# Kernel tuning notes

Hardware: AMD Instinct MI355X
Metric: run time of the kernel (lower is better)

Reference implementation:

```python
import jax, jax.numpy as jnp
import numpy as np

B, S, V, E, H, L = 32, 512, 32000, 256, 512, 48


def setup_inputs() -> dict:
    key = jax.random.key(0)
    ks = jax.random.split(key, 12)
    tokens = jax.random.randint(ks[0], (B, S), 0, V)
    length = jax.random.randint(ks[1], (B,), S // 2, S + 1)
    labels = jax.random.randint(ks[2], (B, S), 0, L)
    embed_table = jax.random.normal(ks[3], (V, E), jnp.float32) * 0.1
    embed_table = embed_table.at[0].set(0.0)  # padding_idx = 0
    # torch LSTM gate order: i, f, g, o ; b = b_ih + b_hh folded together
    w_ih_f = jax.random.normal(ks[4], (4 * H, E), jnp.float32) * 0.05
    w_hh_f = jax.random.normal(ks[5], (4 * H, H), jnp.float32) * 0.05
    b_f = jnp.zeros((4 * H,), jnp.float32)
    w_ih_b = jax.random.normal(ks[6], (4 * H, E), jnp.float32) * 0.05
    w_hh_b = jax.random.normal(ks[7], (4 * H, H), jnp.float32) * 0.05
    b_b = jnp.zeros((4 * H,), jnp.float32)
    w_em = jax.random.normal(ks[8], (L, 2 * H), jnp.float32) * 0.02
    b_em = jnp.zeros((L,), jnp.float32)
    transition = jax.random.uniform(ks[9], (L, L), jnp.float32)  # torch.rand init
    return {"tokens": tokens, "length": length, "labels": labels,
            "embed_table": embed_table,
            "w_ih_f": w_ih_f, "w_hh_f": w_hh_f, "b_f": b_f,
            "w_ih_b": w_ih_b, "w_hh_b": w_hh_b, "b_b": b_b,
            "w_em": w_em, "b_em": b_em, "transition": transition}


def _lstm_dir(x, w_ih, w_hh, b, reverse):
    # x: [B,S,E] -> hidden states [B,S,H]
    xw = jnp.einsum('bse,ge->bsg', x, w_ih) + b  # precompute input projection [B,S,4H]
    if reverse:
        xw = xw[:, ::-1]
    Bn = x.shape[0]
    Hn = w_hh.shape[1]
    h0 = jnp.zeros((Bn, Hn), x.dtype)
    c0 = jnp.zeros((Bn, Hn), x.dtype)

    def step(carry, xt):
        h, c = carry
        gates = xt + h @ w_hh.T  # [B,4H]
        i, f, g, o = jnp.split(gates, 4, axis=-1)
        i = jax.nn.sigmoid(i)
        f = jax.nn.sigmoid(f)
        g = jnp.tanh(g)
        o = jax.nn.sigmoid(o)
        c = f * c + i * g
        h = o * jnp.tanh(c)
        return (h, c), h

    _, hs = jax.lax.scan(step, (h0, c0), jnp.swapaxes(xw, 0, 1))
    hs = jnp.swapaxes(hs, 0, 1)  # [B,S,H]
    if reverse:
        hs = hs[:, ::-1]
    return hs


def reference(tokens, length, labels, embed_table,
              w_ih_f, w_hh_f, b_f, w_ih_b, w_hh_b, b_b,
              w_em, b_em, transition):
    x = embed_table[tokens]                      # [B,S,E]
    hf = _lstm_dir(x, w_ih_f, w_hh_f, b_f, reverse=False)
    hb = _lstm_dir(x, w_ih_b, w_hh_b, b_b, reverse=True)
    h = jnp.concatenate([hf, hb], axis=-1)       # [B,S,2H]
    logits = jnp.einsum('bsh,lh->bsl', h, w_em) + b_em
    e = jnp.exp(logits)                          # emission = exp(linear), as in source
    T = jnp.exp(transition)                      # transition = exp(param), as in source
    Bn, Sn = tokens.shape
    pos = jnp.arange(Sn)[None, :]
    mask = pos < length[:, None]                 # [B,S] valid positions

    # gold path score: sum emissions over valid steps + transitions between them
    em_real = jnp.take_along_axis(e, labels[..., None], axis=-1)[..., 0]  # [B,S]
    real = jnp.sum(em_real * mask, axis=-1)
    trans_real = T[labels[:, :-1], labels[:, 1:]]                          # [B,S-1]
    real = real + jnp.sum(trans_real * mask[:, 1:], axis=-1)

    # forward algorithm, exactly as written in source:
    # alpha_new[k] = logsumexp_l( alpha[k] + T[k,l] + e_t[l] )
    alpha0 = e[:, 0, :]                          # [B,L]

    def step(alpha, inp):
        et, mt = inp                             # [B,L], [B]
        scores = alpha[:, :, None] + T[None, :, :] + et[:, None, :]  # [B,L,L]
        new = jax.nn.logsumexp(scores, axis=-1)
        alpha = jnp.where(mt[:, None], new, alpha)
        return alpha, None

    alpha, _ = jax.lax.scan(step, alpha0,
                            (jnp.swapaxes(e[:, 1:], 0, 1),
                             jnp.swapaxes(mask[:, 1:], 0, 1)))
    sum_score = jax.nn.logsumexp(alpha, axis=-1)  # [B]
    return sum_score - real                       # negative log probability per example
```

## Files before the change

kernel.cpp:

```cpp
#include <hip/hip_runtime.h>
#include <math.h>
#include <stdint.h>

#define Bn 32
#define Sn 512
#define En 256
#define Hn 512
#define Ln 48
#define G4 2048
#define NWG 32
#define SENT16 0x7FFFu

typedef unsigned short u16;
typedef __attribute__((ext_vector_type(8))) __bf16 bf16x8;
typedef __attribute__((ext_vector_type(4))) float f32x4;

__device__ inline float bf2f(u16 u) {
    return __uint_as_float(((unsigned)u) << 16);
}
__device__ inline u16 f2bf(float f) {
    unsigned u = __float_as_uint(f);
    unsigned r = (u + 0x7fffu + ((u >> 16) & 1u)) >> 16;
    return (u16)r;
}
__device__ inline float sigmoidf_(float x) { return 1.f / (1.f + expf(-x)); }
__device__ inline float tanh_fast(float x) { return 2.f / (1.f + expf(-2.f * x)) - 1.f; }

__device__ inline unsigned badMask(f32x4 v) {
    unsigned acc = 0;
    #pragma unroll
    for (int i = 0; i < 4; i++) {
        unsigned d = __float_as_uint(v[i]);
        unsigned x = d ^ 0x7FFF7FFFu;
        acc |= (x - 0x00010001u) & ~x & 0x80008000u;
    }
    return acc;
}

__global__ __launch_bounds__(256) void prep_kernel(
    const int* __restrict__ tokens, const float* __restrict__ embed,
    const float* __restrict__ wihf, const float* __restrict__ wihb,
    const float* __restrict__ whhf, const float* __restrict__ whhb,
    const float* __restrict__ wem, const float* __restrict__ trans,
    u16* __restrict__ xbf, u16* __restrict__ wihf_b, u16* __restrict__ wihb_b,
    u16* __restrict__ whhf_b, u16* __restrict__ whhb_b, u16* __restrict__ wem_b,
    float* __restrict__ expT, float* __restrict__ alphaAcc,
    float* __restrict__ realAcc, unsigned* __restrict__ hf32,
    unsigned* __restrict__ hb32)
{
    size_t idx = (size_t)blockIdx.x * blockDim.x + threadIdx.x;
    size_t stride = (size_t)gridDim.x * blockDim.x;
    for (size_t i = idx; i < (size_t)Bn * Sn * En; i += stride) {
        size_t n = i >> 8; int ee = (int)(i & 255);
        int tok = tokens[n];
        xbf[i] = f2bf(embed[(size_t)tok * En + ee]);
    }
    for (size_t i = idx; i < (size_t)G4 * En; i += stride) {
        wihf_b[i] = f2bf(wihf[i]); wihb_b[i] = f2bf(wihb[i]);
    }
    for (size_t i = idx; i < (size_t)G4 * Hn; i += stride) {
        whhf_b[i] = f2bf(whhf[i]); whhb_b[i] = f2bf(whhb[i]);
    }
    for (size_t i = idx; i < (size_t)Ln * 2 * Hn; i += stride) wem_b[i] = f2bf(wem[i]);
    for (size_t i = idx; i < (size_t)Ln * Ln; i += stride) expT[i] = expf(trans[i]);
    for (size_t i = idx; i < (size_t)Bn * Ln; i += stride) alphaAcc[i] = 0.f;
    for (size_t i = idx; i < (size_t)Bn; i += stride) realAcc[i] = 0.f;
    const unsigned sp = (SENT16 << 16) | SENT16;
    for (size_t i = idx; i < (size_t)Bn * Sn * Hn / 2; i += stride) {
        hf32[i] = sp; hb32[i] = sp;
    }
}

__global__ __launch_bounds__(256) void gemm_xw(
    const u16* __restrict__ xbf, const u16* __restrict__ wihf_b,
    const u16* __restrict__ wihb_b, const float* __restrict__ bias_f,
    const float* __restrict__ bias_b, u16* __restrict__ xw_f, u16* __restrict__ xw_b)
{
    int mb = blockIdx.x, nb = blockIdx.y, dir = blockIdx.z;
    const u16* wih = dir ? wihb_b : wihf_b;
    const float* bias = dir ? bias_b : bias_f;
    u16* xw = dir ? xw_b : xw_f;

    __shared__ u16 At[64 * 136];
    __shared__ u16 Bt[64 * 136];

    int tid = threadIdx.x;
    int w = tid >> 6, lane = tid & 63;
    int lm = lane & 15, lkq = (lane >> 4) * 8;
    int Moff = (w & 1) * 32, Noff = (w >> 1) * 32;

    f32x4 zero = {0.f, 0.f, 0.f, 0.f};
    f32x4 acc[2][2] = {{zero, zero}, {zero, zero}};

    for (int kc = 0; kc < 2; kc++) {
        for (int c = tid; c < 1024; c += 256) {
            int r = c >> 4, cc = (c & 15) * 8;
            *(bf16x8*)&At[r * 136 + cc] =
                *(const bf16x8*)&xbf[((size_t)(mb * 64 + r)) * En + kc * 128 + cc];
            *(bf16x8*)&Bt[r * 136 + cc] =
                *(const bf16x8*)&wih[((size_t)(nb * 64 + r)) * En + kc * 128 + cc];
        }
        __syncthreads();
        #pragma unroll
        for (int ks = 0; ks < 4; ks++) {
            int k = ks * 32 + lkq;
            bf16x8 a0 = *(const bf16x8*)&At[(Moff + lm) * 136 + k];
            bf16x8 a1 = *(const bf16x8*)&At[(Moff + 16 + lm) * 136 + k];
            bf16x8 b0 = *(const bf16x8*)&Bt[(Noff + lm) * 136 + k];
            bf16x8 b1 = *(const bf16x8*)&Bt[(Noff + 16 + lm) * 136 + k];
            acc[0][0] = __builtin_amdgcn_mfma_f32_16x16x32_bf16(a0, b0, acc[0][0], 0, 0, 0);
            acc[0][1] = __builtin_amdgcn_mfma_f32_16x16x32_bf16(a0, b1, acc[0][1], 0, 0, 0);
            acc[1][0] = __builtin_amdgcn_mfma_f32_16x16x32_bf16(a1, b0, acc[1][0], 0, 0, 0);
            acc[1][1] = __builtin_amdgcn_mfma_f32_16x16x32_bf16(a1, b1, acc[1][1], 0, 0, 0);
        }
        __syncthreads();
    }
    #pragma unroll
    for (int mi = 0; mi < 2; mi++)
        #pragma unroll
        for (int ni = 0; ni < 2; ni++)
            #pragma unroll
            for (int reg = 0; reg < 4; reg++) {
                int row = Moff + mi * 16 + (lane >> 4) * 4 + reg;
                int col = Noff + ni * 16 + lm;
                int n = mb * 64 + row;
                int g = nb * 64 + col;
                int t = n & 511, b = n >> 9;
                float v = acc[mi][ni][reg] + bias[g];
                xw[((size_t)t * Bn + b) * G4 + g] = f2bf(v);
            }
}

__global__ __launch_bounds__(512) void lstm_rec(
    const u16* __restrict__ whhf_b, const u16* __restrict__ whhb_b,
    const u16* __restrict__ xw_f, const u16* __restrict__ xw_b,
    u16* __restrict__ hf, u16* __restrict__ hb)
{
    int wg = blockIdx.x;
    int dir = wg >> 5;
    int w = wg & 31;
    const u16* __restrict__ whh = dir ? whhb_b : whhf_b;
    const u16* __restrict__ xw  = dir ? xw_b  : xw_f;
    u16* __restrict__ hbuf = dir ? hb : hf;

    __shared__ u16 Hs[32 * 512];
    __shared__ float Cp[4 * 32 * 17];
    __shared__ u16 hout[32 * 16];

    int tid = threadIdx.x;
    int wv = tid >> 6, lane = tid & 63;
    int lm = lane & 15, kq = lane >> 4;
    int mt = wv & 1, nt = wv >> 1;
    int b = tid >> 4, hc = tid & 15;

    bf16x8 Bf[16];
    {
        const u16* wrow = &whh[((size_t)nt * Hn + (size_t)w * 16 + lm) * Hn];
        #pragma unroll
        for (int ks = 0; ks < 16; ks++)
            Bf[ks] = *(const bf16x8*)&wrow[ks * 32 + kq * 8];
    }

    float c_state = 0.f;
    const f32x4 zero = {0.f, 0.f, 0.f, 0.f};

    for (int it = 0; it < Sn; it++) {
        int t = dir ? (Sn - 1 - it) : it;
        f32x4 acc = zero;

        const u16* xp = &xw[((size_t)t * Bn + b) * G4 + (size_t)w * 16 + hc];
        float xg0 = bf2f(xp[0 * Hn]);
        float xg1 = bf2f(xp[1 * Hn]);
        float xg2 = bf2f(xp[2 * Hn]);
        float xg3 = bf2f(xp[3 * Hn]);

        if (it > 0) {
            int tprev = dir ? (t + 1) : (t - 1);
            const u16* base = &hbuf[((size_t)b * Sn + tprev) * Hn];
            const u16* p0 = base + (hc + 0) * 8;
            const u16* p1 = base + (hc + 16) * 8;
            const u16* p2 = base + (hc + 32) * 8;
            const u16* p3 = base + (hc + 48) * 8;
            f32x4 h0, h1, h2, h3;
            int tries = 0;
            while (true) {
                asm volatile(
                    "global_load_dwordx4 %0, %4, off sc1\n\t"
                    "global_load_dwordx4 %1, %5, off sc1\n\t"
                    "global_load_dwordx4 %2, %6, off sc1\n\t"
                    "global_load_dwordx4 %3, %7, off sc1\n\t"
                    "s_waitcnt vmcnt(0)"
                    : "=v"(h0), "=v"(h1), "=v"(h2), "=v"(h3)
                    : "v"(p0), "v"(p1), "v"(p2), "v"(p3)
                    : "memory");
                if (!(badMask(h0) | badMask(h1) | badMask(h2) | badMask(h3))) break;
                if (++tries > (1 << 16)) break;
            }
            *(f32x4*)&Hs[(b * 64 + ((hc + 0) ^ (b & 7))) * 8] = h0;
            *(f32x4*)&Hs[(b * 64 + ((hc + 16) ^ (b & 7))) * 8] = h1;
            *(f32x4*)&Hs[(b * 64 + ((hc + 32) ^ (b & 7))) * 8] = h2;
            *(f32x4*)&Hs[(b * 64 + ((hc + 48) ^ (b & 7))) * 8] = h3;
            __syncthreads();

            f32x4 aa = zero, ab = zero;
            #pragma unroll
            for (int ks2 = 0; ks2 < 8; ks2++) {
                bf16x8 a0 = *(const bf16x8*)
                    &Hs[((mt * 16 + lm) * 64 + (((2 * ks2) * 4 + kq) ^ (lm & 7))) * 8];
                aa = __builtin_amdgcn_mfma_f32_16x16x32_bf16(a0, Bf[2 * ks2], aa, 0, 0, 0);
                bf16x8 a1 = *(const bf16x8*)
                    &Hs[((mt * 16 + lm) * 64 + (((2 * ks2 + 1) * 4 + kq) ^ (lm & 7))) * 8];
                ab = __builtin_amdgcn_mfma_f32_16x16x32_bf16(a1, Bf[2 * ks2 + 1], ab, 0, 0, 0);
            }
            acc = aa + ab;
        }

        #pragma unroll
        for (int reg = 0; reg < 4; reg++)
            Cp[(nt * 32 + mt * 16 + kq * 4 + reg) * 17 + lm] = acc[reg];
        __syncthreads();

        float g0 = Cp[(0 * 32 + b) * 17 + hc] + xg0;
        float g1 = Cp[(1 * 32 + b) * 17 + hc] + xg1;
        float g2 = Cp[(2 * 32 + b) * 17 + hc] + xg2;
        float g3 = Cp[(3 * 32 + b) * 17 + hc] + xg3;
        float i_ = sigmoidf_(g0);
        float f_ = sigmoidf_(g1);
        float gg = tanh_fast(g2);
        float o_ = sigmoidf_(g3);
        c_state = f_ * c_state + i_ * gg;
        float hv = o_ * tanh_fast(c_state);
        hout[tid] = f2bf(hv);
        __syncthreads();

        if (tid < 64) {
            int bq = lane >> 1, half = lane & 1;
            f32x4 hv8 = *(const f32x4*)&hout[lane * 8];
            u16* sp = &hbuf[((size_t)bq * Sn + t) * Hn + (size_t)w * 16 + half * 8];
            asm volatile("global_store_dwordx4 %0, %1, off sc1"
                         :: "v"(sp), "v"(hv8) : "memory");
        }
    }
}

__global__ __launch_bounds__(256) void emis(
    const u16* __restrict__ hf, const u16* __restrict__ hb,
    const u16* __restrict__ wem_b, const float* __restrict__ bem,
    float* __restrict__ e)
{
    int mb = blockIdx.x;
    int tid = threadIdx.x, wv = tid >> 6, lane = tid & 63;
    int lm = lane & 15, lkq = (lane >> 4) * 8;
    int row = mb * 64 + wv * 16;

    f32x4 zero = {0.f, 0.f, 0.f, 0.f};
    f32x4 acc[3] = {zero, zero, zero};
    for (int ks = 0; ks < 32; ks++) {
        int k = ks * 32 + lkq;
        const u16* hsrc = (ks < 16) ? &hf[(size_t)(row + lm) * Hn + k]
                                    : &hb[(size_t)(row + lm) * Hn + (k - 512)];
        bf16x8 a = *(const bf16x8*)hsrc;
        #pragma unroll
        for (int nt = 0; nt < 3; nt++) {
            bf16x8 bfr = *(const bf16x8*)&wem_b[(size_t)(nt * 16 + lm) * 1024 + k];
            acc[nt] = __builtin_amdgcn_mfma_f32_16x16x32_bf16(a, bfr, acc[nt], 0, 0, 0);
        }
    }
    #pragma unroll
    for (int nt = 0; nt < 3; nt++)
        #pragma unroll
        for (int reg = 0; reg < 4; reg++) {
            int r = row + (lane >> 4) * 4 + reg;
            int col = nt * 16 + lm;
            float lg = acc[nt][reg] + bem[col];
            e[(size_t)r * Ln + col] = expf(lg);
        }
}

__global__ __launch_bounds__(64) void crf_step(
    const float* __restrict__ e, const float* __restrict__ expT,
    const int* __restrict__ labels, const int* __restrict__ lengths,
    float* __restrict__ alphaAcc, float* __restrict__ realAcc)
{
    int bt = blockIdx.x;
    int b = bt >> 9, t = bt & 511;
    __shared__ float er[Ln];
    int tid = threadIdx.x;
    if (tid < Ln) er[tid] = e[(size_t)bt * Ln + tid];
    __syncthreads();
    bool inlen = t < lengths[b];
    if (t >= 1 && inlen && tid < Ln) {
        int i = tid;
        float m = -1e30f;
        for (int j = 0; j < Ln; j++) m = fmaxf(m, expT[i * Ln + j] + er[j]);
        float s = 0.f;
        for (int j = 0; j < Ln; j++) s += expf(expT[i * Ln + j] + er[j] - m);
        atomicAdd(&alphaAcc[b * Ln + i], m + logf(s));
    }
    if (tid == 0 && inlen) {
        int lab = labels[b * Sn + t];
        float r = er[lab];
        if (t >= 1) r += expT[labels[b * Sn + t - 1] * Ln + lab];
        atomicAdd(&realAcc[b], r);
    }
}

__global__ __launch_bounds__(64) void finalize(
    const float* __restrict__ e, const float* __restrict__ alphaAcc,
    const float* __restrict__ realAcc, float* __restrict__ out)
{
    int b = threadIdx.x;
    if (b >= Bn) return;
    float m = -1e30f;
    for (int i = 0; i < Ln; i++) {
        float a = e[((size_t)b * Sn) * Ln + i] + alphaAcc[b * Ln + i];
        m = fmaxf(m, a);
    }
    float s = 0.f;
    for (int i = 0; i < Ln; i++) {
        float a = e[((size_t)b * Sn) * Ln + i] + alphaAcc[b * Ln + i];
        s += expf(a - m);
    }
    out[b] = m + logf(s) - realAcc[b];
}

extern "C" void kernel_launch(void* const* d_in, const int* in_sizes, int n_in,
                              void* d_out, int out_size, void* d_ws, size_t ws_size,
                              hipStream_t stream)
{
    const int*   tokens = (const int*)d_in[0];
    const int*   length = (const int*)d_in[1];
    const int*   labels = (const int*)d_in[2];
    const float* embed  = (const float*)d_in[3];
    const float* wihf   = (const float*)d_in[4];
    const float* whhf   = (const float*)d_in[5];
    const float* bf     = (const float*)d_in[6];
    const float* wihb   = (const float*)d_in[7];
    const float* whhb   = (const float*)d_in[8];
    const float* bbv    = (const float*)d_in[9];
    const float* wem    = (const float*)d_in[10];
    const float* bem    = (const float*)d_in[11];
    const float* trans  = (const float*)d_in[12];
    float* out = (float*)d_out;

    char* p = (char*)d_ws;
    auto take = [&](size_t bytes) -> char* {
        char* q = p;
        p += (bytes + 255) & ~(size_t)255;
        return q;
    };
    u16* xw_f   = (u16*)take((size_t)Sn * Bn * G4 * 2);
    u16* xw_b   = (u16*)take((size_t)Sn * Bn * G4 * 2);
    u16* hf     = (u16*)take((size_t)Bn * Sn * Hn * 2);
    u16* hb     = (u16*)take((size_t)Bn * Sn * Hn * 2);
    u16* xbf    = (u16*)take((size_t)Bn * Sn * En * 2);
    u16* wihf_b = (u16*)take((size_t)G4 * En * 2);
    u16* wihb_b = (u16*)take((size_t)G4 * En * 2);
    u16* whhf_b = (u16*)take((size_t)G4 * Hn * 2);
    u16* whhb_b = (u16*)take((size_t)G4 * Hn * 2);
    u16* wem_b  = (u16*)take((size_t)Ln * 2 * Hn * 2);
    float* e        = (float*)take((size_t)Bn * Sn * Ln * 4);
    float* expT     = (float*)take((size_t)Ln * Ln * 4);
    float* alphaAcc = (float*)take((size_t)Bn * Ln * 4);
    float* realAcc  = (float*)take((size_t)Bn * 4);
    if ((size_t)(p - (char*)d_ws) > ws_size) return;

    prep_kernel<<<4096, 256, 0, stream>>>(tokens, embed, wihf, wihb, whhf, whhb, wem, trans,
                                          xbf, wihf_b, wihb_b, whhf_b, whhb_b, wem_b,
                                          expT, alphaAcc, realAcc,
                                          (unsigned*)hf, (unsigned*)hb);

    dim3 g1(256, 32, 2);
    gemm_xw<<<g1, 256, 0, stream>>>(xbf, wihf_b, wihb_b, bf, bbv, xw_f, xw_b);

    void* ra[] = { (void*)&whhf_b, (void*)&whhb_b, (void*)&xw_f, (void*)&xw_b,
                   (void*)&hf, (void*)&hb };
    hipLaunchCooperativeKernel((const void*)lstm_rec, dim3(2 * NWG), dim3(512), ra, 0, stream);

    emis<<<256, 256, 0, stream>>>(hf, hb, wem_b, bem, e);
    crf_step<<<Bn * Sn, 64, 0, stream>>>(e, expT, labels, length, alphaAcc, realAcc);
    finalize<<<1, 64, 0, stream>>>(e, alphaAcc, realAcc, out);
}
```

Before: 1.890 ms.

## Load MFMA A-fragments of h directly from global, dropping LDS staging and barrier

Changes the hidden-state buffer layout from [B,S,H] to [S,B,H] so each wave can fetch its MFMA A operands for the previous timestep straight from global memory with sixteen offset loads. This removes the LDS staging copy and one __syncthreads per timestep on the serial recurrence path. The emission kernel's output indexing is remapped so the CRF stage still sees [B,S,L]. In exchange each wave issues more global loads per step, some of them redundant across waves, and the spin-poll now checks sixteen vectors.

```diff
diff --git a/kernel.cpp b/kernel.cpp
--- a/kernel.cpp
+++ b/kernel.cpp
@@ -143,7 +143,6 @@
     const u16* __restrict__ xw  = dir ? xw_b  : xw_f;
     u16* __restrict__ hbuf = dir ? hb : hf;
 
-    __shared__ u16 Hs[32 * 512];
     __shared__ float Cp[4 * 32 * 17];
     __shared__ u16 hout[32 * 16];
 
@@ -176,43 +175,58 @@
 
         if (it > 0) {
             int tprev = dir ? (t + 1) : (t - 1);
-            const u16* base = &hbuf[((size_t)b * Sn + tprev) * Hn];
-            const u16* p0 = base + (hc + 0) * 8;
-            const u16* p1 = base + (hc + 16) * 8;
-            const u16* p2 = base + (hc + 32) * 8;
-            const u16* p3 = base + (hc + 48) * 8;
-            f32x4 h0, h1, h2, h3;
+            const u16* ab = &hbuf[((size_t)tprev * Bn + (size_t)(mt * 16 + lm)) * Hn + kq * 8];
+            f32x4 A0, A1, A2, A3, A4, A5, A6, A7, A8, A9, A10, A11, A12, A13, A14, A15;
             int tries = 0;
             while (true) {
                 asm volatile(
-                    "global_load_dwordx4 %0, %4, off sc1\n\t"
-                    "global_load_dwordx4 %1, %5, off sc1\n\t"
-                    "global_load_dwordx4 %2, %6, off sc1\n\t"
-                    "global_load_dwordx4 %3, %7, off sc1\n\t"
+                    "global_load_dwordx4 %0, %16, off sc1\n\t"
+                    "global_load_dwordx4 %1, %16, off offset:64 sc1\n\t"
+                    "global_load_dwordx4 %2, %16, off offset:128 sc1\n\t"
+                    "global_load_dwordx4 %3, %16, off offset:192 sc1\n\t"
+                    "global_load_dwordx4 %4, %16, off offset:256 sc1\n\t"
+                    "global_load_dwordx4 %5, %16, off offset:320 sc1\n\t"
+                    "global_load_dwordx4 %6, %16, off offset:384 sc1\n\t"
+                    "global_load_dwordx4 %7, %16, off offset:448 sc1\n\t"
+                    "global_load_dwordx4 %8, %16, off offset:512 sc1\n\t"
+                    "global_load_dwordx4 %9, %16, off offset:576 sc1\n\t"
+                    "global_load_dwordx4 %10, %16, off offset:640 sc1\n\t"
+                    "global_load_dwordx4 %11, %16, off offset:704 sc1\n\t"
+                    "global_load_dwordx4 %12, %16, off offset:768 sc1\n\t"
+                    "global_load_dwordx4 %13, %16, off offset:832 sc1\n\t"
+                    "global_load_dwordx4 %14, %16, off offset:896 sc1\n\t"
+                    "global_load_dwordx4 %15, %16, off offset:960 sc1\n\t"
                     "s_waitcnt vmcnt(0)"
-                    : "=v"(h0), "=v"(h1), "=v"(h2), "=v"(h3)
-                    : "v"(p0), "v"(p1), "v"(p2), "v"(p3)
-                    : "memory");
-                if (!(badMask(h0) | badMask(h1) | badMask(h2) | badMask(h3))) break;
+                    : "=v"(A0), "=v"(A1), "=v"(A2), "=v"(A3),
+                      "=v"(A4), "=v"(A5), "=v"(A6), "=v"(A7),
+                      "=v"(A8), "=v"(A9), "=v"(A10), "=v"(A11),
+                      "=v"(A12), "=v"(A13), "=v"(A14), "=v"(A15)
+                    : "v"(ab) : "memory");
+                unsigned bad = badMask(A0) | badMask(A1) | badMask(A2) | badMask(A3)
+                             | badMask(A4) | badMask(A5) | badMask(A6) | badMask(A7)
+                             | badMask(A8) | badMask(A9) | badMask(A10) | badMask(A11)
+                             | badMask(A12) | badMask(A13) | badMask(A14) | badMask(A15);
+                if (!bad) break;
                 if (++tries > (1 << 16)) break;
             }
-            *(f32x4*)&Hs[(b * 64 + ((hc + 0) ^ (b & 7))) * 8] = h0;
-            *(f32x4*)&Hs[(b * 64 + ((hc + 16) ^ (b & 7))) * 8] = h1;
-            *(f32x4*)&Hs[(b * 64 + ((hc + 32) ^ (b & 7))) * 8] = h2;
-            *(f32x4*)&Hs[(b * 64 + ((hc + 48) ^ (b & 7))) * 8] = h3;
-            __syncthreads();
-
-            f32x4 aa = zero, ab = zero;
-            #pragma unroll
-            for (int ks2 = 0; ks2 < 8; ks2++) {
-                bf16x8 a0 = *(const bf16x8*)
-                    &Hs[((mt * 16 + lm) * 64 + (((2 * ks2) * 4 + kq) ^ (lm & 7))) * 8];
-                aa = __builtin_amdgcn_mfma_f32_16x16x32_bf16(a0, Bf[2 * ks2], aa, 0, 0, 0);
-                bf16x8 a1 = *(const bf16x8*)
-                    &Hs[((mt * 16 + lm) * 64 + (((2 * ks2 + 1) * 4 + kq) ^ (lm & 7))) * 8];
-                ab = __builtin_amdgcn_mfma_f32_16x16x32_bf16(a1, Bf[2 * ks2 + 1], ab, 0, 0, 0);
-            }
-            acc = aa + ab;
+            f32x4 aa = zero, ab2 = zero;
+            aa  = __builtin_amdgcn_mfma_f32_16x16x32_bf16(*(bf16x8*)&A0,  Bf[0],  aa,  0, 0, 0);
+            ab2 = __builtin_amdgcn_mfma_f32_16x16x32_bf16(*(bf16x8*)&A1,  Bf[1],  ab2, 0, 0, 0);
+            aa  = __builtin_amdgcn_mfma_f32_16x16x32_bf16(*(bf16x8*)&A2,  Bf[2],  aa,  0, 0, 0);
+            ab2 = __builtin_amdgcn_mfma_f32_16x16x32_bf16(*(bf16x8*)&A3,  Bf[3],  ab2, 0, 0, 0);
+            aa  = __builtin_amdgcn_mfma_f32_16x16x32_bf16(*(bf16x8*)&A4,  Bf[4],  aa,  0, 0, 0);
+            ab2 = __builtin_amdgcn_mfma_f32_16x16x32_bf16(*(bf16x8*)&A5,  Bf[5],  ab2, 0, 0, 0);
+            aa  = __builtin_amdgcn_mfma_f32_16x16x32_bf16(*(bf16x8*)&A6,  Bf[6],  aa,  0, 0, 0);
+            ab2 = __builtin_amdgcn_mfma_f32_16x16x32_bf16(*(bf16x8*)&A7,  Bf[7],  ab2, 0, 0, 0);
+            aa  = __builtin_amdgcn_mfma_f32_16x16x32_bf16(*(bf16x8*)&A8,  Bf[8],  aa,  0, 0, 0);
+            ab2 = __builtin_amdgcn_mfma_f32_16x16x32_bf16(*(bf16x8*)&A9,  Bf[9],  ab2, 0, 0, 0);
+            aa  = __builtin_amdgcn_mfma_f32_16x16x32_bf16(*(bf16x8*)&A10, Bf[10], aa,  0, 0, 0);
+            ab2 = __builtin_amdgcn_mfma_f32_16x16x32_bf16(*(bf16x8*)&A11, Bf[11], ab2, 0, 0, 0);
+            aa  = __builtin_amdgcn_mfma_f32_16x16x32_bf16(*(bf16x8*)&A12, Bf[12], aa,  0, 0, 0);
+            ab2 = __builtin_amdgcn_mfma_f32_16x16x32_bf16(*(bf16x8*)&A13, Bf[13], ab2, 0, 0, 0);
+            aa  = __builtin_amdgcn_mfma_f32_16x16x32_bf16(*(bf16x8*)&A14, Bf[14], aa,  0, 0, 0);
+            ab2 = __builtin_amdgcn_mfma_f32_16x16x32_bf16(*(bf16x8*)&A15, Bf[15], ab2, 0, 0, 0);
+            acc = aa + ab2;
         }
 
         #pragma unroll
@@ -236,7 +250,7 @@
         if (tid < 64) {
             int bq = lane >> 1, half = lane & 1;
             f32x4 hv8 = *(const f32x4*)&hout[lane * 8];
-            u16* sp = &hbuf[((size_t)bq * Sn + t) * Hn + (size_t)w * 16 + half * 8];
+            u16* sp = &hbuf[((size_t)t * Bn + bq) * Hn + (size_t)w * 16 + half * 8];
             asm volatile("global_store_dwordx4 %0, %1, off sc1"
                          :: "v"(sp), "v"(hv8) : "memory");
         }
@@ -272,8 +286,9 @@
         for (int reg = 0; reg < 4; reg++) {
             int r = row + (lane >> 4) * 4 + reg;
             int col = nt * 16 + lm;
+            int bb = r & 31, tt = r >> 5;
             float lg = acc[nt][reg] + bem[col];
-            e[(size_t)r * Ln + col] = expf(lg);
+            e[(((size_t)bb << 9) + tt) * Ln + col] = expf(lg);
         }
 }
 
```

New measurement: 3.749 ms. 98.4% more time.

## Halve recurrent LSTM workgroups, each handling 32 hidden units per step

Applied to the files above, without the earlier changes.

The persistent recurrent kernel now uses 16 workgroups per direction instead of 32. Each workgroup owns 32 hidden columns, holds two sets of W_hh fragments in registers and issues twice the MFMAs per step. Fewer workgroups means fewer participants polling each step's h broadcast through global memory, which should cut synchronisation latency. The cost is more register pressure and about twice the per-step compute and gate math per workgroup. The host launch grid must also shrink to match.

```diff
diff --git a/kernel.cpp b/kernel.cpp
--- a/kernel.cpp
+++ b/kernel.cpp
@@ -8,7 +8,7 @@
 #define Hn 512
 #define Ln 48
 #define G4 2048
-#define NWG 32
+#define NWG 16
 #define SENT16 0x7FFFu
 
 typedef unsigned short u16;
@@ -137,15 +137,15 @@
     u16* __restrict__ hf, u16* __restrict__ hb)
 {
     int wg = blockIdx.x;
-    int dir = wg >> 5;
-    int w = wg & 31;
+    int dir = wg >> 4;
+    int w = wg & 15;
     const u16* __restrict__ whh = dir ? whhb_b : whhf_b;
     const u16* __restrict__ xw  = dir ? xw_b  : xw_f;
     u16* __restrict__ hbuf = dir ? hb : hf;
 
     __shared__ u16 Hs[32 * 512];
-    __shared__ float Cp[4 * 32 * 17];
-    __shared__ u16 hout[32 * 16];
+    __shared__ float Cp[4 * 32 * 33];
+    __shared__ u16 hout[32 * 32];
 
     int tid = threadIdx.x;
     int wv = tid >> 6, lane = tid & 63;
@@ -153,26 +153,29 @@
     int mt = wv & 1, nt = wv >> 1;
     int b = tid >> 4, hc = tid & 15;
 
-    bf16x8 Bf[16];
+    bf16x8 Bf0[16], Bf1[16];
     {
-        const u16* wrow = &whh[((size_t)nt * Hn + (size_t)w * 16 + lm) * Hn];
-        #pragma unroll
-        for (int ks = 0; ks < 16; ks++)
-            Bf[ks] = *(const bf16x8*)&wrow[ks * 32 + kq * 8];
-    }
-
-    float c_state = 0.f;
+        const u16* wrow0 = &whh[((size_t)nt * Hn + (size_t)w * 32 + lm) * Hn];
+        const u16* wrow1 = &whh[((size_t)nt * Hn + (size_t)w * 32 + 16 + lm) * Hn];
+        #pragma unroll
+        for (int ks = 0; ks < 16; ks++) {
+            Bf0[ks] = *(const bf16x8*)&wrow0[ks * 32 + kq * 8];
+            Bf1[ks] = *(const bf16x8*)&wrow1[ks * 32 + kq * 8];
+        }
+    }
+
+    float cs0 = 0.f, cs1 = 0.f;
     const f32x4 zero = {0.f, 0.f, 0.f, 0.f};
 
     for (int it = 0; it < Sn; it++) {
         int t = dir ? (Sn - 1 - it) : it;
-        f32x4 acc = zero;
-
-        const u16* xp = &xw[((size_t)t * Bn + b) * G4 + (size_t)w * 16 + hc];
-        float xg0 = bf2f(xp[0 * Hn]);
-        float xg1 = bf2f(xp[1 * Hn]);
-        float xg2 = bf2f(xp[2 * Hn]);
-        float xg3 = bf2f(xp[3 * Hn]);
+        f32x4 acc0 = zero, acc1 = zero;
+
+        const u16* xp = &xw[((size_t)t * Bn + b) * G4 + (size_t)w * 32 + hc];
+        float xgA0 = bf2f(xp[0 * Hn]),      xgB0 = bf2f(xp[0 * Hn + 16]);
+        float xgA1 = bf2f(xp[1 * Hn]),      xgB1 = bf2f(xp[1 * Hn + 16]);
+        float xgA2 = bf2f(xp[2 * Hn]),      xgB2 = bf2f(xp[2 * Hn + 16]);
+        float xgA3 = bf2f(xp[3 * Hn]),      xgB3 = bf2f(xp[3 * Hn + 16]);
 
         if (it > 0) {
             int tprev = dir ? (t + 1) : (t - 1);
@@ -202,41 +205,54 @@
             *(f32x4*)&Hs[(b * 64 + ((hc + 48) ^ (b & 7))) * 8] = h3;
             __syncthreads();
 
-            f32x4 aa = zero, ab = zero;
+            f32x4 aa0 = zero, ab0 = zero, aa1 = zero, ab1 = zero;
             #pragma unroll
             for (int ks2 = 0; ks2 < 8; ks2++) {
                 bf16x8 a0 = *(const bf16x8*)
                     &Hs[((mt * 16 + lm) * 64 + (((2 * ks2) * 4 + kq) ^ (lm & 7))) * 8];
-                aa = __builtin_amdgcn_mfma_f32_16x16x32_bf16(a0, Bf[2 * ks2], aa, 0, 0, 0);
+                aa0 = __builtin_amdgcn_mfma_f32_16x16x32_bf16(a0, Bf0[2 * ks2], aa0, 0, 0, 0);
+                aa1 = __builtin_amdgcn_mfma_f32_16x16x32_bf16(a0, Bf1[2 * ks2], aa1, 0, 0, 0);
                 bf16x8 a1 = *(const bf16x8*)
                     &Hs[((mt * 16 + lm) * 64 + (((2 * ks2 + 1) * 4 + kq) ^ (lm & 7))) * 8];
-                ab = __builtin_amdgcn_mfma_f32_16x16x32_bf16(a1, Bf[2 * ks2 + 1], ab, 0, 0, 0);
+                ab0 = __builtin_amdgcn_mfma_f32_16x16x32_bf16(a1, Bf0[2 * ks2 + 1], ab0, 0, 0, 0);
+                ab1 = __builtin_amdgcn_mfma_f32_16x16x32_bf16(a1, Bf1[2 * ks2 + 1], ab1, 0, 0, 0);
             }
-            acc = aa + ab;
-        }
-
-        #pragma unroll
-        for (int reg = 0; reg < 4; reg++)
-            Cp[(nt * 32 + mt * 16 + kq * 4 + reg) * 17 + lm] = acc[reg];
+            acc0 = aa0 + ab0;
+            acc1 = aa1 + ab1;
+        }
+
+        #pragma unroll
+        for (int reg = 0; reg < 4; reg++) {
+            int r = (nt * 32 + mt * 16 + kq * 4 + reg) * 33;
+            Cp[r + lm] = acc0[reg];
+            Cp[r + 16 + lm] = acc1[reg];
+        }
         __syncthreads();
 
-        float g0 = Cp[(0 * 32 + b) * 17 + hc] + xg0;
-        float g1 = Cp[(1 * 32 + b) * 17 + hc] + xg1;
-        float g2 = Cp[(2 * 32 + b) * 17 + hc] + xg2;
-        float g3 = Cp[(3 * 32 + b) * 17 + hc] + xg3;
-        float i_ = sigmoidf_(g0);
-        float f_ = sigmoidf_(g1);
-        float gg = tanh_fast(g2);
-        float o_ = sigmoidf_(g3);
-        c_state = f_ * c_state + i_ * gg;
-        float hv = o_ * tanh_fast(c_state);
-        hout[tid] = f2bf(hv);
+        float gA0 = Cp[(0 * 32 + b) * 33 + hc] + xgA0;
+        float gA1 = Cp[(1 * 32 + b) * 33 + hc] + xgA1;
+        float gA2 = Cp[(2 * 32 + b) * 33 + hc] + xgA2;
+        float gA3 = Cp[(3 * 32 + b) * 33 + hc] + xgA3;
+        float gB0 = Cp[(0 * 32 + b) * 33 + 16 + hc] + xgB0;
+        float gB1 = Cp[(1 * 32 + b) * 33 + 16 + hc] + xgB1;
+        float gB2 = Cp[(2 * 32 + b) * 33 + 16 + hc] + xgB2;
+        float gB3 = Cp[(3 * 32 + b) * 33 + 16 + hc] + xgB3;
+        float iA = sigmoidf_(gA0), fA = sigmoidf_(gA1);
+        float gA = tanh_fast(gA2), oA = sigmoidf_(gA3);
+        cs0 = fA * cs0 + iA * gA;
+        float hvA = oA * tanh_fast(cs0);
+        float iB = sigmoidf_(gB0), fB = sigmoidf_(gB1);
+        float gB = tanh_fast(gB2), oB = sigmoidf_(gB3);
+        cs1 = fB * cs1 + iB * gB;
+        float hvB = oB * tanh_fast(cs1);
+        hout[b * 32 + hc] = f2bf(hvA);
+        hout[b * 32 + 16 + hc] = f2bf(hvB);
         __syncthreads();
 
-        if (tid < 64) {
-            int bq = lane >> 1, half = lane & 1;
-            f32x4 hv8 = *(const f32x4*)&hout[lane * 8];
-            u16* sp = &hbuf[((size_t)bq * Sn + t) * Hn + (size_t)w * 16 + half * 8];
+        if (tid < 128) {
+            int bq = tid >> 2, part = tid & 3;
+            f32x4 hv8 = *(const f32x4*)&hout[bq * 32 + part * 8];
+            u16* sp = &hbuf[((size_t)bq * Sn + t) * Hn + (size_t)w * 32 + part * 8];
             asm volatile("global_store_dwordx4 %0, %1, off sc1"
                          :: "v"(sp), "v"(hv8) : "memory");
         }
```

Result: no change. 1.918 ms (+1.5%).

## Fuse emission GEMM with CRF step and enlarge xw GEMM tiles

Applied to the files above, without the earlier changes.

The emission kernel now keeps each block's 64 timesteps of emissions in shared memory and computes the CRF logsumexp terms and gold-path scores in place. It reduces these per block before issuing atomics, so the separate 16K-block crf_step launch and the full emission buffer round-trip are gone; only the t=0 emissions are written out for finalize. Separately, the input-projection GEMM moves from 64x64 to 128x128 tiles with a 4x4 MFMA accumulator grid per wave, increasing reuse at the cost of more registers and fewer blocks. These stages are small next to the sequential LSTM recurrence, so the overall effect is likely limited.

```diff
diff --git a/kernel.cpp b/kernel.cpp
--- a/kernel.cpp
+++ b/kernel.cpp
@@ -81,50 +81,61 @@
     const float* bias = dir ? bias_b : bias_f;
     u16* xw = dir ? xw_b : xw_f;
 
-    __shared__ u16 At[64 * 136];
-    __shared__ u16 Bt[64 * 136];
+    __shared__ u16 As[128 * 72];
+    __shared__ u16 Bs[128 * 72];
 
     int tid = threadIdx.x;
     int w = tid >> 6, lane = tid & 63;
-    int lm = lane & 15, lkq = (lane >> 4) * 8;
-    int Moff = (w & 1) * 32, Noff = (w >> 1) * 32;
+    int lm = lane & 15, kq = lane >> 4;
+    int Moff = (w & 1) * 64, Noff = (w >> 1) * 64;
 
     f32x4 zero = {0.f, 0.f, 0.f, 0.f};
-    f32x4 acc[2][2] = {{zero, zero}, {zero, zero}};
-
-    for (int kc = 0; kc < 2; kc++) {
-        for (int c = tid; c < 1024; c += 256) {
-            int r = c >> 4, cc = (c & 15) * 8;
-            *(bf16x8*)&At[r * 136 + cc] =
-                *(const bf16x8*)&xbf[((size_t)(mb * 64 + r)) * En + kc * 128 + cc];
-            *(bf16x8*)&Bt[r * 136 + cc] =
-                *(const bf16x8*)&wih[((size_t)(nb * 64 + r)) * En + kc * 128 + cc];
+    f32x4 acc[4][4];
+    #pragma unroll
+    for (int mi = 0; mi < 4; mi++)
+        #pragma unroll
+        for (int ni = 0; ni < 4; ni++) acc[mi][ni] = zero;
+
+    for (int kc = 0; kc < 4; kc++) {
+        #pragma unroll
+        for (int it = 0; it < 4; it++) {
+            int idx = tid + it * 256;
+            int r = idx >> 3, pos = (idx & 7) * 8;
+            *(bf16x8*)&As[r * 72 + pos] =
+                *(const bf16x8*)&xbf[((size_t)(mb * 128 + r)) * En + kc * 64 + pos];
+            *(bf16x8*)&Bs[r * 72 + pos] =
+                *(const bf16x8*)&wih[((size_t)(nb * 128 + r)) * En + kc * 64 + pos];
         }
         __syncthreads();
         #pragma unroll
-        for (int ks = 0; ks < 4; ks++) {
-            int k = ks * 32 + lkq;
-            bf16x8 a0 = *(const bf16x8*)&At[(Moff + lm) * 136 + k];
-            bf16x8 a1 = *(const bf16x8*)&At[(Moff + 16 + lm) * 136 + k];
-            bf16x8 b0 = *(const bf16x8*)&Bt[(Noff + lm) * 136 + k];
-            bf16x8 b1 = *(const bf16x8*)&Bt[(Noff + 16 + lm) * 136 + k];
-            acc[0][0] = __builtin_amdgcn_mfma_f32_16x16x32_bf16(a0, b0, acc[0][0], 0, 0, 0);
-            acc[0][1] = __builtin_amdgcn_mfma_f32_16x16x32_bf16(a0, b1, acc[0][1], 0, 0, 0);
-            acc[1][0] = __builtin_amdgcn_mfma_f32_16x16x32_bf16(a1, b0, acc[1][0], 0, 0, 0);
-            acc[1][1] = __builtin_amdgcn_mfma_f32_16x16x32_bf16(a1, b1, acc[1][1], 0, 0, 0);
+        for (int ks = 0; ks < 2; ks++) {
+            int k = ks * 32 + kq * 8;
+            bf16x8 af[4], bfr[4];
+            #pragma unroll
+            for (int mi = 0; mi < 4; mi++)
+                af[mi] = *(const bf16x8*)&As[(Moff + mi * 16 + lm) * 72 + k];
+            #pragma unroll
+            for (int ni = 0; ni < 4; ni++)
+                bfr[ni] = *(const bf16x8*)&Bs[(Noff + ni * 16 + lm) * 72 + k];
+            #pragma unroll
+            for (int mi = 0; mi < 4; mi++)
+                #pragma unroll
+                for (int ni = 0; ni < 4; ni++)
+                    acc[mi][ni] = __builtin_amdgcn_mfma_f32_16x16x32_bf16(
+                        af[mi], bfr[ni], acc[mi][ni], 0, 0, 0);
         }
         __syncthreads();
     }
     #pragma unroll
-    for (int mi = 0; mi < 2; mi++)
-        #pragma unroll
-        for (int ni = 0; ni < 2; ni++)
+    for (int mi = 0; mi < 4; mi++)
+        #pragma unroll
+        for (int ni = 0; ni < 4; ni++)
             #pragma unroll
             for (int reg = 0; reg < 4; reg++) {
-                int row = Moff + mi * 16 + (lane >> 4) * 4 + reg;
+                int row = Moff + mi * 16 + kq * 4 + reg;
                 int col = Noff + ni * 16 + lm;
-                int n = mb * 64 + row;
-                int g = nb * 64 + col;
+                int n = mb * 128 + row;
+                int g = nb * 128 + col;
                 int t = n & 511, b = n >> 9;
                 float v = acc[mi][ni][reg] + bias[g];
                 xw[((size_t)t * Bn + b) * G4 + g] = f2bf(v);
@@ -243,13 +254,25 @@
     }
 }
 
-__global__ __launch_bounds__(256) void emis(
+__global__ __launch_bounds__(256) void emis_crf(
     const u16* __restrict__ hf, const u16* __restrict__ hb,
     const u16* __restrict__ wem_b, const float* __restrict__ bem,
-    float* __restrict__ e)
+    const float* __restrict__ expT, const int* __restrict__ labels,
+    const int* __restrict__ lengths, float* __restrict__ e0,
+    float* __restrict__ alphaAcc, float* __restrict__ realAcc)
 {
     int mb = blockIdx.x;
-    int tid = threadIdx.x, wv = tid >> 6, lane = tid & 63;
+    int b = mb >> 3, t0 = (mb & 7) * 64;
+
+    __shared__ float eL[64][49];
+    __shared__ float Ts[48 * 48];
+    __shared__ float sred[4][48];
+    __shared__ float rred[64];
+
+    int tid = threadIdx.x;
+    for (int i = tid; i < 48 * 48; i += 256) Ts[i] = expT[i];
+
+    int wv = tid >> 6, lane = tid & 63;
     int lm = lane & 15, lkq = (lane >> 4) * 8;
     int row = mb * 64 + wv * 16;
 
@@ -270,55 +293,65 @@
     for (int nt = 0; nt < 3; nt++)
         #pragma unroll
         for (int reg = 0; reg < 4; reg++) {
-            int r = row + (lane >> 4) * 4 + reg;
+            int rib = wv * 16 + (lane >> 4) * 4 + reg;
             int col = nt * 16 + lm;
-            float lg = acc[nt][reg] + bem[col];
-            e[(size_t)r * Ln + col] = expf(lg);
-        }
-}
-
-__global__ __launch_bounds__(64) void crf_step(
-    const float* __restrict__ e, const float* __restrict__ expT,
-    const int* __restrict__ labels, const int* __restrict__ lengths,
-    float* __restrict__ alphaAcc, float* __restrict__ realAcc)
-{
-    int bt = blockIdx.x;
-    int b = bt >> 9, t = bt & 511;
-    __shared__ float er[Ln];
-    int tid = threadIdx.x;
-    if (tid < Ln) er[tid] = e[(size_t)bt * Ln + tid];
+            float v = expf(acc[nt][reg] + bem[col]);
+            eL[rib][col] = v;
+            if ((mb & 7) == 0 && rib == 0) e0[b * Ln + col] = v;
+        }
     __syncthreads();
-    bool inlen = t < lengths[b];
-    if (t >= 1 && inlen && tid < Ln) {
-        int i = tid;
-        float m = -1e30f;
-        for (int j = 0; j < Ln; j++) m = fmaxf(m, expT[i * Ln + j] + er[j]);
-        float s = 0.f;
-        for (int j = 0; j < Ln; j++) s += expf(expT[i * Ln + j] + er[j] - m);
-        atomicAdd(&alphaAcc[b * Ln + i], m + logf(s));
-    }
-    if (tid == 0 && inlen) {
-        int lab = labels[b * Sn + t];
-        float r = er[lab];
-        if (t >= 1) r += expT[labels[b * Sn + t - 1] * Ln + lab];
+
+    int len = lengths[b];
+    if (tid < 192) {
+        int i = tid % 48, tg = tid / 48;
+        float sacc = 0.f;
+        for (int p = tg * 16; p < tg * 16 + 16; p++) {
+            int t = t0 + p;
+            if (t >= 1 && t < len) {
+                float m = -1e30f;
+                for (int j = 0; j < 48; j++) m = fmaxf(m, Ts[i * 48 + j] + eL[p][j]);
+                float s = 0.f;
+                for (int j = 0; j < 48; j++) s += expf(Ts[i * 48 + j] + eL[p][j] - m);
+                sacc += m + logf(s);
+            }
+        }
+        sred[tg][i] = sacc;
+    } else {
+        int p = tid - 192;
+        int t = t0 + p;
+        float r = 0.f;
+        if (t < len) {
+            int lab = labels[b * Sn + t];
+            r = eL[p][lab];
+            if (t >= 1) r += Ts[labels[b * Sn + t - 1] * 48 + lab];
+        }
+        rred[p] = r;
+    }
+    __syncthreads();
+    if (tid < 48) {
+        float s = sred[0][tid] + sred[1][tid] + sred[2][tid] + sred[3][tid];
+        atomicAdd(&alphaAcc[b * Ln + tid], s);
+    } else if (tid == 48) {
+        float r = 0.f;
+        for (int p = 0; p < 64; p++) r += rred[p];
         atomicAdd(&realAcc[b], r);
     }
 }
 
 __global__ __launch_bounds__(64) void finalize(
-    const float* __restrict__ e, const float* __restrict__ alphaAcc,
+    const float* __restrict__ e0, const float* __restrict__ alphaAcc,
     const float* __restrict__ realAcc, float* __restrict__ out)
 {
     int b = threadIdx.x;
     if (b >= Bn) return;
     float m = -1e30f;
     for (int i = 0; i < Ln; i++) {
-        float a = e[((size_t)b * Sn) * Ln + i] + alphaAcc[b * Ln + i];
+        float a = e0[b * Ln + i] + alphaAcc[b * Ln + i];
         m = fmaxf(m, a);
     }
     float s = 0.f;
     for (int i = 0; i < Ln; i++) {
-        float a = e[((size_t)b * Sn) * Ln + i] + alphaAcc[b * Ln + i];
+        float a = e0[b * Ln + i] + alphaAcc[b * Ln + i];
         s += expf(a - m);
     }
     out[b] = m + logf(s) - realAcc[b];
@@ -359,8 +392,8 @@
     u16* whhf_b = (u16*)take((size_t)G4 * Hn * 2);
     u16* whhb_b = (u16*)take((size_t)G4 * Hn * 2);
     u16* wem_b  = (u16*)take((size_t)Ln * 2 * Hn * 2);
-    float* e        = (float*)take((size_t)Bn * Sn * Ln * 4);
     float* expT     = (float*)take((size_t)Ln * Ln * 4);
+    float* e0       = (float*)take((size_t)Bn * Ln * 4);
     float* alphaAcc = (float*)take((size_t)Bn * Ln * 4);
     float* realAcc  = (float*)take((size_t)Bn * 4);
     if ((size_t)(p - (char*)d_ws) > ws_size) return;
@@ -370,14 +403,14 @@
                                           expT, alphaAcc, realAcc,
                                           (unsigned*)hf, (unsigned*)hb);
 
-    dim3 g1(256, 32, 2);
+    dim3 g1(128, 16, 2);
     gemm_xw<<<g1, 256, 0, stream>>>(xbf, wihf_b, wihb_b, bf, bbv, xw_f, xw_b);
 
     void* ra[] = { (void*)&whhf_b, (void*)&whhb_b, (void*)&xw_f, (void*)&xw_b,
                    (void*)&hf, (void*)&hb };
     hipLaunchCooperativeKernel((const void*)lstm_rec, dim3(2 * NWG), dim3(512), ra, 0, stream);
 
-    emis<<<256, 256, 0, stream>>>(hf, hb, wem_b, bem, e);
-    crf_step<<<Bn * Sn, 64, 0, stream>>>(e, expT, labels, length, alphaAcc, realAcc);
-    finalize<<<1, 64, 0, stream>>>(e, alphaAcc, realAcc, out);
-}
+    emis_crf<<<256, 256, 0, stream>>>(hf, hb, wem_b, bem, expT, labels, length,
+                                      e0, alphaAcc, realAcc);
+    finalize<<<1, 64, 0, stream>>>(e0, alphaAcc, realAcc, out);
+}
```

Result: faster. 1.801 ms (-4.7%).
